# Optimization experiments

Measured on AMD Instinct MI355X. Metric: run time of the kernel, lower is better.

The kernel has to match this reference:

```python
import jax, jax.numpy as jnp
import numpy as np

BINS = 64
EPS = 1e-8


def _compute_histogram(gray, bins=BINS):
    # gray: [B, H, W] -> normalized histogram [B, bins]
    B = gray.shape[0]
    flat = gray.reshape(B, -1)                      # [B, N]
    mn = flat.min(axis=1, keepdims=True)
    mx = flat.max(axis=1, keepdims=True)
    valid = mx > mn                                  # [B, 1]
    norm = (flat - mn) / jnp.where(valid, mx - mn, 1.0)
    idx = jnp.clip((norm * (bins - 1)).astype(jnp.int32), 0, bins - 1)  # [B, N]
    # per-image bincount via scatter-add
    hist = jax.vmap(lambda i: jnp.zeros(bins, dtype=flat.dtype).at[i].add(1.0))(idx)
    hist = hist / hist.sum(axis=1, keepdims=True)
    return jnp.where(valid, hist, jnp.full_like(hist, 1.0 / bins))


def reference(x, y, lambda_cc=10.0):
    # channel balance
    x_mean = jnp.mean(x, axis=(2, 3), keepdims=True)   # [B,3,1,1]
    y_mean = jnp.mean(y, axis=(2, 3), keepdims=True)
    x_bal = x_mean / (jnp.sum(x_mean, axis=1, keepdims=True) + EPS)
    y_bal = y_mean / (jnp.sum(y_mean, axis=1, keepdims=True) + EPS)
    color_balance_loss = jnp.mean(jnp.abs(x_bal - y_bal))

    # luminance
    x_gray = 0.299 * x[:, 0] + 0.587 * x[:, 1] + 0.114 * x[:, 2]  # [B,H,W]
    y_gray = 0.299 * y[:, 0] + 0.587 * y[:, 1] + 0.114 * y[:, 2]

    x_hist = _compute_histogram(x_gray)
    y_hist = _compute_histogram(y_gray)

    # F.kl_div(log(x_hist+eps), y_hist, reduction='batchmean')
    log_in = jnp.log(x_hist + EPS)
    ylogy = jnp.where(y_hist > 0, y_hist * jnp.log(jnp.where(y_hist > 0, y_hist, 1.0)), 0.0)
    kl = jnp.sum(ylogy - y_hist * log_in) / x.shape[0]

    return lambda_cc * (color_balance_loss + kl)


def setup_inputs() -> dict:
    key = jax.random.key(0)
    k1, k2 = jax.random.split(key)
    x = jax.random.uniform(k1, (16, 3, 512, 512), dtype=jnp.float32)
    y = jax.random.uniform(k2, (16, 3, 512, 512), dtype=jnp.float32)
    return {"x": x, "y": y}
```

## Files before the change

kernel.cpp:

```cpp
#include <hip/hip_runtime.h>

#define HW_N (512 * 512)
#define BINS 64
#define BPI  64
#define TPB  256
#define QPB  ((HW_N / 4) / BPI)
#define MAXB 16

struct Part {
    double sum[6];
    float  mn[2];
    float  mx[2];
};

__device__ __forceinline__ unsigned int f2ord(float f) {
    unsigned int u = __float_as_uint(f);
    return (u & 0x80000000u) ? ~u : (u | 0x80000000u);
}

__device__ __forceinline__ float grayf(float r, float g, float b) {
    return 0.299f * r + 0.587f * g + 0.114f * b;
}

__device__ __forceinline__ double waveSumD(double v) {
#pragma unroll
    for (int o = 32; o > 0; o >>= 1) v += __shfl_down(v, o);
    return v;
}
__device__ __forceinline__ float waveMinAll(float v) {
#pragma unroll
    for (int o = 32; o > 0; o >>= 1) v = fminf(v, __shfl_xor(v, o));
    return v;
}
__device__ __forceinline__ float waveMaxAll(float v) {
#pragma unroll
    for (int o = 32; o > 0; o >>= 1) v = fmaxf(v, __shfl_xor(v, o));
    return v;
}

__global__ __launch_bounds__(TPB) void k_pass1(const float* __restrict__ x,
                                               const float* __restrict__ y,
                                               Part* __restrict__ part,
                                               unsigned int* __restrict__ img_hist,
                                               float* __restrict__ gx,
                                               float* __restrict__ gy) {
    const int tid = threadIdx.x;
    const int blk = blockIdx.x;
    const int b   = blk / BPI;
    const int sub = blk % BPI;

    if (sub == 0)
        for (int i = tid; i < 2 * BINS; i += TPB) img_hist[b * 2 * BINS + i] = 0u;

    const int q0 = sub * QPB;
    const size_t base = (size_t)b * 3 * HW_N;

    const float4* xr = (const float4*)(x + base);
    const float4* xg = (const float4*)(x + base + HW_N);
    const float4* xb = (const float4*)(x + base + 2 * HW_N);
    const float4* yr = (const float4*)(y + base);
    const float4* yg = (const float4*)(y + base + HW_N);
    const float4* yb = (const float4*)(y + base + 2 * HW_N);
    float4* gxp = (float4*)(gx + (size_t)b * HW_N);
    float4* gyp = (float4*)(gy + (size_t)b * HW_N);

    float s0 = 0.f, s1 = 0.f, s2 = 0.f;
    float t0 = 0.f, t1 = 0.f, t2 = 0.f;
    float mnx = 3.4e38f, mxx = -3.4e38f;
    float mny = 3.4e38f, mxy = -3.4e38f;

    for (int i = tid; i < QPB; i += TPB) {
        const int q = q0 + i;
        float4 r = xr[q], g = xg[q], bl = xb[q];
        s0 += (r.x + r.y) + (r.z + r.w);
        s1 += (g.x + g.y) + (g.z + g.w);
        s2 += (bl.x + bl.y) + (bl.z + bl.w);
        {
            float g0 = grayf(r.x, g.x, bl.x), g1 = grayf(r.y, g.y, bl.y);
            float g2 = grayf(r.z, g.z, bl.z), g3 = grayf(r.w, g.w, bl.w);
            mnx = fminf(mnx, fminf(fminf(g0, g1), fminf(g2, g3)));
            mxx = fmaxf(mxx, fmaxf(fmaxf(g0, g1), fmaxf(g2, g3)));
            gxp[q] = make_float4(g0, g1, g2, g3);
        }
        r = yr[q]; g = yg[q]; bl = yb[q];
        t0 += (r.x + r.y) + (r.z + r.w);
        t1 += (g.x + g.y) + (g.z + g.w);
        t2 += (bl.x + bl.y) + (bl.z + bl.w);
        {
            float g0 = grayf(r.x, g.x, bl.x), g1 = grayf(r.y, g.y, bl.y);
            float g2 = grayf(r.z, g.z, bl.z), g3 = grayf(r.w, g.w, bl.w);
            mny = fminf(mny, fminf(fminf(g0, g1), fminf(g2, g3)));
            mxy = fmaxf(mxy, fmaxf(fmaxf(g0, g1), fmaxf(g2, g3)));
            gyp[q] = make_float4(g0, g1, g2, g3);
        }
    }

    const int wave = tid >> 6;
    const int lane = tid & 63;
    __shared__ double shs[6][TPB / 64];
    __shared__ float  shmn[2][TPB / 64];
    __shared__ float  shmx[2][TPB / 64];

    double d;
    d = waveSumD((double)s0); if (!lane) shs[0][wave] = d;
    d = waveSumD((double)s1); if (!lane) shs[1][wave] = d;
    d = waveSumD((double)s2); if (!lane) shs[2][wave] = d;
    d = waveSumD((double)t0); if (!lane) shs[3][wave] = d;
    d = waveSumD((double)t1); if (!lane) shs[4][wave] = d;
    d = waveSumD((double)t2); if (!lane) shs[5][wave] = d;
    float f;
    f = waveMinAll(mnx); if (!lane) shmn[0][wave] = f;
    f = waveMinAll(mny); if (!lane) shmn[1][wave] = f;
    f = waveMaxAll(mxx); if (!lane) shmx[0][wave] = f;
    f = waveMaxAll(mxy); if (!lane) shmx[1][wave] = f;
    __syncthreads();

    if (tid == 0) {
        Part& p = part[blk];
        p.sum[0] = shs[0][0] + shs[0][1] + shs[0][2] + shs[0][3];
        p.sum[1] = shs[1][0] + shs[1][1] + shs[1][2] + shs[1][3];
        p.sum[2] = shs[2][0] + shs[2][1] + shs[2][2] + shs[2][3];
        p.sum[3] = shs[3][0] + shs[3][1] + shs[3][2] + shs[3][3];
        p.sum[4] = shs[4][0] + shs[4][1] + shs[4][2] + shs[4][3];
        p.sum[5] = shs[5][0] + shs[5][1] + shs[5][2] + shs[5][3];
        p.mn[0] = fminf(fminf(shmn[0][0], shmn[0][1]), fminf(shmn[0][2], shmn[0][3]));
        p.mn[1] = fminf(fminf(shmn[1][0], shmn[1][1]), fminf(shmn[1][2], shmn[1][3]));
        p.mx[0] = fmaxf(fmaxf(shmx[0][0], shmx[0][1]), fmaxf(shmx[0][2], shmx[0][3]));
        p.mx[1] = fmaxf(fmaxf(shmx[1][0], shmx[1][1]), fmaxf(shmx[1][2], shmx[1][3]));
    }
}

__global__ __launch_bounds__(TPB) void k_pass2(const float* __restrict__ gx,
                                               const float* __restrict__ gy,
                                               const Part* __restrict__ part,
                                               unsigned int* __restrict__ img_hist) {
    const int tid = threadIdx.x;
    const int blk = blockIdx.x;
    const int b   = blk / BPI;
    const int sub = blk % BPI;
    const int wave = tid >> 6;
    const int lane = tid & 63;

    const float4 mm = *(const float4*)&part[b * BPI + lane].mn[0];
    const float imnx = waveMinAll(mm.x);
    const float imny = waveMinAll(mm.y);
    const float imxx = waveMaxAll(mm.z);
    const float imxy = waveMaxAll(mm.w);
    const float rgx = (imxx > imnx) ? (imxx - imnx) : 1.0f;
    const float rgy = (imxy > imny) ? (imxy - imny) : 1.0f;

    __shared__ unsigned int lh[8][BINS];
    for (int i = tid; i < 8 * BINS; i += TPB) ((unsigned int*)lh)[i] = 0u;
    __syncthreads();

    const int q0 = sub * QPB;
    const float4* gxp = (const float4*)(gx + (size_t)b * HW_N);
    const float4* gyp = (const float4*)(gy + (size_t)b * HW_N);

    unsigned int* hx = lh[wave];
    unsigned int* hy = lh[4 + wave];

    for (int i = tid; i < QPB; i += TPB) {
        const int q = q0 + i;
        {
            const float4 gv = gxp[q];
            const float g[4] = { gv.x, gv.y, gv.z, gv.w };
#pragma unroll
            for (int j = 0; j < 4; j++) {
                float t = ((g[j] - imnx) / rgx) * 63.0f;
                int id = (int)t;
                id = id < 0 ? 0 : (id > 63 ? 63 : id);
                atomicAdd(&hx[id], 1u);
            }
        }
        {
            const float4 gv = gyp[q];
            const float g[4] = { gv.x, gv.y, gv.z, gv.w };
#pragma unroll
            for (int j = 0; j < 4; j++) {
                float t = ((g[j] - imny) / rgy) * 63.0f;
                int id = (int)t;
                id = id < 0 ? 0 : (id > 63 ? 63 : id);
                atomicAdd(&hy[id], 1u);
            }
        }
    }
    __syncthreads();

    for (int i = tid; i < 2 * BINS; i += TPB) {
        const int src = i >> 6, bin = i & 63;
        unsigned int v = lh[src * 4 + 0][bin] + lh[src * 4 + 1][bin] +
                         lh[src * 4 + 2][bin] + lh[src * 4 + 3][bin];
        if (v) atomicAdd(&img_hist[(b * 2 + src) * BINS + bin], v);
    }
}

__global__ __launch_bounds__(1024) void k_final(const Part* __restrict__ part,
                                                const unsigned int* __restrict__ img_hist,
                                                float* __restrict__ out, int B) {
    const int tid = threadIdx.x;

    __shared__ double ssum[MAXB][6];
    __shared__ unsigned int somn[MAXB][2], somx[MAXB][2];
    __shared__ double skl[16], scb[16];

    for (int t = tid; t < B * 6; t += 1024) {
        const int bb = t / 6, k = t - bb * 6;
        double a = 0.0;
#pragma unroll 8
        for (int s = 0; s < BPI; s++) a += part[bb * BPI + s].sum[k];
        ssum[bb][k] = a;
    }
    for (int t = tid; t < MAXB * 2; t += 1024) {
        somn[t >> 1][t & 1] = 0xFFFFFFFFu;
        somx[t >> 1][t & 1] = 0u;
    }
    __syncthreads();
    for (int t = tid; t < B * BPI; t += 1024) {
        const int bb = t / BPI;
        const float4 mm = *(const float4*)&part[t].mn[0];
        atomicMin(&somn[bb][0], f2ord(mm.x));
        atomicMin(&somn[bb][1], f2ord(mm.y));
        atomicMax(&somx[bb][0], f2ord(mm.z));
        atomicMax(&somx[bb][1], f2ord(mm.w));
    }
    __syncthreads();

    const float invN = 1.0f / (float)HW_N;
    double klt = 0.0, cbt = 0.0;

    for (int t = tid; t < B * BINS; t += 1024) {
        const int bb = t >> 6, bin = t & 63;
        const bool vldx = somx[bb][0] > somn[bb][0];
        const bool vldy = somx[bb][1] > somn[bb][1];
        const float xh = vldx ? (float)img_hist[(bb * 2 + 0) * BINS + bin] * invN : (1.0f / BINS);
        const float yh = vldy ? (float)img_hist[(bb * 2 + 1) * BINS + bin] * invN : (1.0f / BINS);
        const float log_in = logf(xh + 1e-8f);
        const float ylogy = (yh > 0.0f) ? yh * logf(yh) : 0.0f;
        klt += (double)ylogy - (double)yh * (double)log_in;
    }

    for (int t = tid; t < B * 3; t += 1024) {
        const int bb = t / 3, c = t - bb * 3;
        const double N = (double)HW_N;
        const double xbal = (ssum[bb][c] / N) /
                            ((ssum[bb][0] + ssum[bb][1] + ssum[bb][2]) / N + 1e-8);
        const double ybal = (ssum[bb][3 + c] / N) /
                            ((ssum[bb][3] + ssum[bb][4] + ssum[bb][5]) / N + 1e-8);
        cbt += fabs(xbal - ybal);
    }

    const double kw = waveSumD(klt);
    const double cw = waveSumD(cbt);
    const int wave = tid >> 6, lane = tid & 63;
    if (!lane) { skl[wave] = kw; scb[wave] = cw; }
    __syncthreads();
    if (tid == 0) {
        double K = 0.0, C = 0.0;
        for (int i = 0; i < 16; i++) { K += skl[i]; C += scb[i]; }
        const double kl = K / (double)B;
        const double cb = C / (double)(B * 3);
        out[0] = (float)(10.0 * (cb + kl));
    }
}

extern "C" void kernel_launch(void* const* d_in, const int* in_sizes, int n_in,
                              void* d_out, int out_size, void* d_ws, size_t ws_size,
                              hipStream_t stream) {
    const float* x = (const float*)d_in[0];
    const float* y = (const float*)d_in[1];
    float* out = (float*)d_out;
    const int B = in_sizes[0] / (3 * HW_N);

    char* ws = (char*)d_ws;
    Part* part = (Part*)ws;
    unsigned int* img_hist = (unsigned int*)(ws + (size_t)B * BPI * sizeof(Part));
    float* gx = (float*)(ws + (1 << 20));
    float* gy = gx + (size_t)B * HW_N;

    k_pass1<<<B * BPI, TPB, 0, stream>>>(x, y, part, img_hist, gx, gy);
    k_pass2<<<B * BPI, TPB, 0, stream>>>(gx, gy, part, img_hist);
    k_final<<<1, 1024, 0, stream>>>(part, img_hist, out, B);
}
```

Measured before the change: 142.7 us.

## Fuse final reduction into histogram pass using last-block atomic counters

Removes the separate single-block final kernel. The last block to finish each image's histogram pass now computes that image's KL and color-balance terms and adds them to global double accumulators. A second counter lets the last image write the output. This saves one kernel launch and the serialized single-block tail, at the cost of atomic counters, memory-ordering handling, and a nondeterministic floating-point summation order.

```diff
diff --git a/kernel.cpp b/kernel.cpp
--- a/kernel.cpp
+++ b/kernel.cpp
@@ -13,10 +13,13 @@
     float  mx[2];
 };
 
-__device__ __forceinline__ unsigned int f2ord(float f) {
-    unsigned int u = __float_as_uint(f);
-    return (u & 0x80000000u) ? ~u : (u | 0x80000000u);
-}
+struct Ctrl {
+    unsigned int done[MAXB];
+    unsigned int done2;
+    unsigned int pad[3];
+    double klacc;
+    double cbacc;
+};
 
 __device__ __forceinline__ float grayf(float r, float g, float b) {
     return 0.299f * r + 0.587f * g + 0.114f * b;
@@ -42,6 +45,7 @@
                                                const float* __restrict__ y,
                                                Part* __restrict__ part,
                                                unsigned int* __restrict__ img_hist,
+                                               unsigned int* __restrict__ ctrl_w,
                                                float* __restrict__ gx,
                                                float* __restrict__ gy) {
     const int tid = threadIdx.x;
@@ -51,6 +55,7 @@
 
     if (sub == 0)
         for (int i = tid; i < 2 * BINS; i += TPB) img_hist[b * 2 * BINS + i] = 0u;
+    if (blk == 0 && tid < sizeof(Ctrl) / 4) ctrl_w[tid] = 0u;
 
     const int q0 = sub * QPB;
     const size_t base = (size_t)b * 3 * HW_N;
@@ -130,10 +135,12 @@
     }
 }
 
-__global__ __launch_bounds__(TPB) void k_pass2(const float* __restrict__ gx,
-                                               const float* __restrict__ gy,
-                                               const Part* __restrict__ part,
-                                               unsigned int* __restrict__ img_hist) {
+__global__ __launch_bounds__(TPB) void k_pass2f(const float* __restrict__ gx,
+                                                const float* __restrict__ gy,
+                                                const Part* __restrict__ part,
+                                                unsigned int* __restrict__ img_hist,
+                                                Ctrl* __restrict__ ctrl,
+                                                float* __restrict__ out, int B) {
     const int tid = threadIdx.x;
     const int blk = blockIdx.x;
     const int b   = blk / BPI;
@@ -193,74 +200,69 @@
                          lh[src * 4 + 2][bin] + lh[src * 4 + 3][bin];
         if (v) atomicAdd(&img_hist[(b * 2 + src) * BINS + bin], v);
     }
-}
-
-__global__ __launch_bounds__(1024) void k_final(const Part* __restrict__ part,
-                                                const unsigned int* __restrict__ img_hist,
-                                                float* __restrict__ out, int B) {
-    const int tid = threadIdx.x;
-
-    __shared__ double ssum[MAXB][6];
-    __shared__ unsigned int somn[MAXB][2], somx[MAXB][2];
-    __shared__ double skl[16], scb[16];
-
-    for (int t = tid; t < B * 6; t += 1024) {
-        const int bb = t / 6, k = t - bb * 6;
-        double a = 0.0;
-#pragma unroll 8
-        for (int s = 0; s < BPI; s++) a += part[bb * BPI + s].sum[k];
-        ssum[bb][k] = a;
-    }
-    for (int t = tid; t < MAXB * 2; t += 1024) {
-        somn[t >> 1][t & 1] = 0xFFFFFFFFu;
-        somx[t >> 1][t & 1] = 0u;
-    }
-    __syncthreads();
-    for (int t = tid; t < B * BPI; t += 1024) {
-        const int bb = t / BPI;
-        const float4 mm = *(const float4*)&part[t].mn[0];
-        atomicMin(&somn[bb][0], f2ord(mm.x));
-        atomicMin(&somn[bb][1], f2ord(mm.y));
-        atomicMax(&somx[bb][0], f2ord(mm.z));
-        atomicMax(&somx[bb][1], f2ord(mm.w));
-    }
+    __syncthreads();
+
+    __shared__ unsigned int s_li;
+    if (tid == 0) {
+        unsigned int old = __hip_atomic_fetch_add(&ctrl->done[b], 1u,
+                                                  __ATOMIC_RELEASE, __HIP_MEMORY_SCOPE_AGENT);
+        s_li = (old == BPI - 1) ? 1u : 0u;
+    }
+    __syncthreads();
+    if (!s_li) return;
+
+    if (tid == 0)
+        (void)__hip_atomic_load(&ctrl->done[b], __ATOMIC_ACQUIRE, __HIP_MEMORY_SCOPE_AGENT);
     __syncthreads();
 
     const float invN = 1.0f / (float)HW_N;
-    double klt = 0.0, cbt = 0.0;
-
-    for (int t = tid; t < B * BINS; t += 1024) {
-        const int bb = t >> 6, bin = t & 63;
-        const bool vldx = somx[bb][0] > somn[bb][0];
-        const bool vldy = somx[bb][1] > somn[bb][1];
-        const float xh = vldx ? (float)img_hist[(bb * 2 + 0) * BINS + bin] * invN : (1.0f / BINS);
-        const float yh = vldy ? (float)img_hist[(bb * 2 + 1) * BINS + bin] * invN : (1.0f / BINS);
+    const bool vldx = imxx > imnx;
+    const bool vldy = imxy > imny;
+
+    if (tid < 64) {
+        const unsigned int cx = __hip_atomic_load(&img_hist[(b * 2 + 0) * BINS + tid],
+                                                  __ATOMIC_RELAXED, __HIP_MEMORY_SCOPE_AGENT);
+        const unsigned int cy = __hip_atomic_load(&img_hist[(b * 2 + 1) * BINS + tid],
+                                                  __ATOMIC_RELAXED, __HIP_MEMORY_SCOPE_AGENT);
+        const float xh = vldx ? (float)cx * invN : (1.0f / BINS);
+        const float yh = vldy ? (float)cy * invN : (1.0f / BINS);
         const float log_in = logf(xh + 1e-8f);
         const float ylogy = (yh > 0.0f) ? yh * logf(yh) : 0.0f;
-        klt += (double)ylogy - (double)yh * (double)log_in;
-    }
-
-    for (int t = tid; t < B * 3; t += 1024) {
-        const int bb = t / 3, c = t - bb * 3;
-        const double N = (double)HW_N;
-        const double xbal = (ssum[bb][c] / N) /
-                            ((ssum[bb][0] + ssum[bb][1] + ssum[bb][2]) / N + 1e-8);
-        const double ybal = (ssum[bb][3 + c] / N) /
-                            ((ssum[bb][3] + ssum[bb][4] + ssum[bb][5]) / N + 1e-8);
-        cbt += fabs(xbal - ybal);
-    }
-
-    const double kw = waveSumD(klt);
-    const double cw = waveSumD(cbt);
-    const int wave = tid >> 6, lane = tid & 63;
-    if (!lane) { skl[wave] = kw; scb[wave] = cw; }
-    __syncthreads();
+        double term = (double)ylogy - (double)yh * (double)log_in;
+        term = waveSumD(term);
+        if (tid == 0) atomicAdd(&ctrl->klacc, term);
+    } else if (tid < 128) {
+        const int l = tid - 64;
+        const double* ps = &part[b * BPI + l].sum[0];
+        double s0 = waveSumD(ps[0]);
+        double s1 = waveSumD(ps[1]);
+        double s2 = waveSumD(ps[2]);
+        double s3 = waveSumD(ps[3]);
+        double s4 = waveSumD(ps[4]);
+        double s5 = waveSumD(ps[5]);
+        if (l == 0) {
+            const double N = (double)HW_N;
+            const double dx = (s0 + s1 + s2) / N + 1e-8;
+            const double dy = (s3 + s4 + s5) / N + 1e-8;
+            double cbt = 0.0;
+            cbt += fabs((s0 / N) / dx - (s3 / N) / dy);
+            cbt += fabs((s1 / N) / dx - (s4 / N) / dy);
+            cbt += fabs((s2 / N) / dx - (s5 / N) / dy);
+            atomicAdd(&ctrl->cbacc, cbt);
+        }
+    }
+    __syncthreads();
+
     if (tid == 0) {
-        double K = 0.0, C = 0.0;
-        for (int i = 0; i < 16; i++) { K += skl[i]; C += scb[i]; }
-        const double kl = K / (double)B;
-        const double cb = C / (double)(B * 3);
-        out[0] = (float)(10.0 * (cb + kl));
+        unsigned int old2 = __hip_atomic_fetch_add(&ctrl->done2, 1u,
+                                                   __ATOMIC_ACQ_REL, __HIP_MEMORY_SCOPE_AGENT);
+        if (old2 == (unsigned)(B - 1)) {
+            const double K = __hip_atomic_load(&ctrl->klacc, __ATOMIC_RELAXED,
+                                               __HIP_MEMORY_SCOPE_AGENT);
+            const double C = __hip_atomic_load(&ctrl->cbacc, __ATOMIC_RELAXED,
+                                               __HIP_MEMORY_SCOPE_AGENT);
+            out[0] = (float)(10.0 * (C / (double)(B * 3) + K / (double)B));
+        }
     }
 }
 
@@ -274,11 +276,12 @@
 
     char* ws = (char*)d_ws;
     Part* part = (Part*)ws;
-    unsigned int* img_hist = (unsigned int*)(ws + (size_t)B * BPI * sizeof(Part));
+    unsigned int* img_hist = (unsigned int*)(ws + 65536);
+    Ctrl* ctrl = (Ctrl*)(ws + 65536 + 8192);
     float* gx = (float*)(ws + (1 << 20));
     float* gy = gx + (size_t)B * HW_N;
 
-    k_pass1<<<B * BPI, TPB, 0, stream>>>(x, y, part, img_hist, gx, gy);
-    k_pass2<<<B * BPI, TPB, 0, stream>>>(gx, gy, part, img_hist);
-    k_final<<<1, 1024, 0, stream>>>(part, img_hist, out, B);
-}
+    k_pass1<<<B * BPI, TPB, 0, stream>>>(x, y, part, img_hist,
+                                         (unsigned int*)ctrl, gx, gy);
+    k_pass2f<<<B * BPI, TPB, 0, stream>>>(gx, gy, part, img_hist, ctrl, out, B);
+}
```

Measured after the change: 158.4 us. 1.11x slower.
